# Kernel optimization log

Hardware: AMD Instinct MI355X
Metric: run time of the kernel (lower is better)

Reference implementation:

```python
import jax, jax.numpy as jnp
import numpy as np

L, D, H, T, B, V, R = 12, 1024, 16, 1024, 2, 50257, 32
HD = D // H
LORA_SCALE = 64.0 / 32.0  # alpha / rank
EPS = 1e-5


def setup_inputs() -> dict:
    key = jax.random.key(0)
    ks = iter(jax.random.split(key, 32))
    f = lambda shape, s=0.02: jax.random.normal(next(ks), shape, dtype=jnp.float32) * s
    inp = {
        'input_ids': jax.random.randint(next(ks), (B, T), 0, V, dtype=jnp.int64),
        'wte': f((V, D)), 'wpe': f((T, D)),
        'ln1_w': jnp.ones((L, D), jnp.float32), 'ln1_b': jnp.zeros((L, D), jnp.float32),
        'attn_w': f((L, 3 * D, D)), 'attn_b': jnp.zeros((L, 3 * D), jnp.float32),
        'attn_la': f((L, R, D), 0.01), 'attn_lb': f((L, 3 * D, R), 0.01),
        'proj_w': f((L, D, D)), 'proj_b': jnp.zeros((L, D), jnp.float32),
        'proj_la': f((L, R, D), 0.01), 'proj_lb': f((L, D, R), 0.01),
        'ln2_w': jnp.ones((L, D), jnp.float32), 'ln2_b': jnp.zeros((L, D), jnp.float32),
        'fc_w': f((L, 4 * D, D)), 'fc_b': jnp.zeros((L, 4 * D), jnp.float32),
        'fc_la': f((L, R, D), 0.01), 'fc_lb': f((L, 4 * D, R), 0.01),
        'mp_w': f((L, D, 4 * D)), 'mp_b': jnp.zeros((L, D), jnp.float32),
        'mp_la': f((L, R, 4 * D), 0.01), 'mp_lb': f((L, D, R), 0.01),
        'lnf_w': jnp.ones((D,), jnp.float32), 'lnf_b': jnp.zeros((D,), jnp.float32),
    }
    return inp


def _ln(x, w, b):
    m = jnp.mean(x, axis=-1, keepdims=True)
    v = jnp.mean(jnp.square(x - m), axis=-1, keepdims=True)
    return (x - m) * jax.lax.rsqrt(v + EPS) * w + b


def _lin(x, W, b, A, Bm):
    # quantized linear at 32-bit (pass-through) + LoRA: x W^T + b + scale * (x A^T) B^T
    return x @ W.T + b + ((x @ A.T) @ Bm.T) * LORA_SCALE


def _forward(input_ids, wte, wpe, ln1_w, ln1_b, attn_w, attn_b, attn_la, attn_lb,
             proj_w, proj_b, proj_la, proj_lb, ln2_w, ln2_b, fc_w, fc_b, fc_la, fc_lb,
             mp_w, mp_b, mp_la, mp_lb, lnf_w, lnf_b):
    Bq, Tq = input_ids.shape
    mask = jnp.tril(jnp.ones((Tq, Tq), dtype=bool))  # causal bias buffer
    h = wte[input_ids] + wpe[jnp.arange(Tq)]  # embed + (eval-mode) dropout

    def blk(h, p):
        l1w, l1b, aw, ab, ala, alb, pw, pb, pla, plb, l2w, l2b, fw, fb, fla, flb, mw, mb, mla, mlb = p
        x = _ln(h, l1w, l1b)
        qkv = _lin(x, aw, ab, ala, alb)  # [B,T,3D]
        q, k, v = jnp.split(qkv, 3, axis=-1)
        q = q.reshape(Bq, Tq, H, HD).transpose(0, 2, 1, 3)
        k = k.reshape(Bq, Tq, H, HD).transpose(0, 2, 1, 3)
        v = v.reshape(Bq, Tq, H, HD).transpose(0, 2, 1, 3)
        s = jnp.einsum('bhqd,bhkd->bhqk', q, k) / jnp.sqrt(jnp.float32(HD))
        s = jnp.where(mask, s, -jnp.inf)
        pa = jax.nn.softmax(s, axis=-1)
        o = jnp.einsum('bhqk,bhkd->bhqd', pa, v).transpose(0, 2, 1, 3).reshape(Bq, Tq, D)
        h = h + _lin(o, pw, pb, pla, plb)
        x = _ln(h, l2w, l2b)
        m = jax.nn.gelu(_lin(x, fw, fb, fla, flb), approximate=False)
        h = h + _lin(m, mw, mb, mla, mlb)
        return h, None

    h, _ = jax.lax.scan(blk, h, (ln1_w, ln1_b, attn_w, attn_b, attn_la, attn_lb,
                                 proj_w, proj_b, proj_la, proj_lb, ln2_w, ln2_b,
                                 fc_w, fc_b, fc_la, fc_lb, mp_w, mp_b, mp_la, mp_lb))
    return _ln(h, lnf_w, lnf_b)


def reference(input_ids, wte, wpe, ln1_w, ln1_b, attn_w, attn_b, attn_la, attn_lb,
              proj_w, proj_b, proj_la, proj_lb, ln2_w, ln2_b, fc_w, fc_b, fc_la, fc_lb,
              mp_w, mp_b, mp_la, mp_lb, lnf_w, lnf_b):
    return _forward(input_ids, wte, wpe, ln1_w, ln1_b, attn_w, attn_b, attn_la, attn_lb,
                    proj_w, proj_b, proj_la, proj_lb, ln2_w, ln2_b, fc_w, fc_b, fc_la, fc_lb,
                    mp_w, mp_b, mp_la, mp_lb, lnf_w, lnf_b)
```

## Files before the change

kernel.cpp:

```cpp
#include <hip/hip_runtime.h>
#include <math.h>

#define TT 1024
#define DD 1024
#define NH 16
#define NB 2
#define NL 12
#define RR 32
#define MM (NB * TT)

typedef __attribute__((ext_vector_type(8))) short bf16x8;
typedef __attribute__((ext_vector_type(4))) float f32x4;

__device__ __forceinline__ unsigned short f2bf(float f) {
  unsigned int u = __float_as_uint(f);
  u = (u + 0x7FFFu + ((u >> 16) & 1u)) >> 16;
  return (unsigned short)u;
}
__device__ __forceinline__ float bf2f(unsigned short u) {
  return __uint_as_float((unsigned int)u << 16);
}

typedef __attribute__((address_space(1))) void gvoid;
typedef __attribute__((address_space(3))) void lvoid;
__device__ __forceinline__ void gload_lds16(const void* g, void* l) {
  __builtin_amdgcn_global_load_lds((gvoid*)g, (lvoid*)l, 16, 0, 0);
}

__global__ __launch_bounds__(256) void embed_cvt_k(
    const int* __restrict__ ids, const float* __restrict__ wte,
    const float* __restrict__ wpe, float* __restrict__ h,
    const float* __restrict__ ala, const float* __restrict__ alb,
    const float* __restrict__ pla, const float* __restrict__ plb,
    const float* __restrict__ fla, const float* __restrict__ flb,
    const float* __restrict__ mla, const float* __restrict__ mlb,
    unsigned short* __restrict__ out) {
  if (blockIdx.x < MM * DD / 256) {
    const int i = blockIdx.x * 256 + threadIdx.x;
    const int row = i >> 10;
    const int d = i & 1023;
    const int t = row & (TT - 1);
    const int id = ids[row];
    h[i] = wte[(size_t)id * DD + d] + wpe[(size_t)t * DD + d];
    return;
  }
  const int g = (blockIdx.x - MM * DD / 256) * 256 + threadIdx.x;
  const int layer = g >> 19;
  const int rem = g & 524287;
  const int row = rem >> 5;
  const int r = rem & 31;
  float v;
  if (row < 1024)       v = ala[(size_t)layer * 32 * 1024 + r * 1024 + row];
  else if (row < 4096)  v = alb[(size_t)layer * 3072 * 32 + (row - 1024) * 32 + r];
  else if (row < 5120)  v = pla[(size_t)layer * 32 * 1024 + r * 1024 + (row - 4096)];
  else if (row < 6144)  v = plb[(size_t)layer * 1024 * 32 + (row - 5120) * 32 + r];
  else if (row < 7168)  v = fla[(size_t)layer * 32 * 1024 + r * 1024 + (row - 6144)];
  else if (row < 11264) v = flb[(size_t)layer * 4096 * 32 + (row - 7168) * 32 + r];
  else if (row < 15360) v = mla[(size_t)layer * 32 * 4096 + r * 4096 + (row - 11264)];
  else                  v = mlb[(size_t)layer * 1024 * 32 + (row - 15360) * 32 + r];
  out[g] = f2bf(v);
}

__global__ __launch_bounds__(256) void ln_bf_k(const float* __restrict__ x,
                                               const float* __restrict__ w,
                                               const float* __restrict__ b,
                                               unsigned short* __restrict__ out) {
  const int row = blockIdx.x;
  const float* xr = x + (size_t)row * DD;
  const float4 v = *(const float4*)(xr + threadIdx.x * 4);
  float s = v.x + v.y + v.z + v.w;
  float ss = v.x * v.x + v.y * v.y + v.z * v.z + v.w * v.w;
#pragma unroll
  for (int off = 32; off > 0; off >>= 1) {
    s += __shfl_down(s, off);
    ss += __shfl_down(ss, off);
  }
  __shared__ float rs[4], rss[4];
  const int wid = threadIdx.x >> 6;
  if ((threadIdx.x & 63) == 0) { rs[wid] = s; rss[wid] = ss; }
  __syncthreads();
  s = rs[0] + rs[1] + rs[2] + rs[3];
  ss = rss[0] + rss[1] + rss[2] + rss[3];
  const float mean = s * (1.f / DD);
  const float var = ss * (1.f / DD) - mean * mean;
  const float rstd = rsqrtf(var + 1e-5f);
  const float4 wv = *(const float4*)(w + threadIdx.x * 4);
  const float4 bv = *(const float4*)(b + threadIdx.x * 4);
  ushort4 o;
  o.x = f2bf((v.x - mean) * rstd * wv.x + bv.x);
  o.y = f2bf((v.y - mean) * rstd * wv.y + bv.y);
  o.z = f2bf((v.z - mean) * rstd * wv.z + bv.z);
  o.w = f2bf((v.w - mean) * rstd * wv.w + bv.w);
  *(ushort4*)(out + (size_t)row * DD + threadIdx.x * 4) = o;
}

__global__ __launch_bounds__(256) void ln_f_k(const float* __restrict__ x,
                                              const float* __restrict__ w,
                                              const float* __restrict__ b,
                                              float* __restrict__ out) {
  const int row = blockIdx.x;
  const float* xr = x + (size_t)row * DD;
  const float4 v = *(const float4*)(xr + threadIdx.x * 4);
  float s = v.x + v.y + v.z + v.w;
  float ss = v.x * v.x + v.y * v.y + v.z * v.z + v.w * v.w;
#pragma unroll
  for (int off = 32; off > 0; off >>= 1) {
    s += __shfl_down(s, off);
    ss += __shfl_down(ss, off);
  }
  __shared__ float rs[4], rss[4];
  const int wid = threadIdx.x >> 6;
  if ((threadIdx.x & 63) == 0) { rs[wid] = s; rss[wid] = ss; }
  __syncthreads();
  s = rs[0] + rs[1] + rs[2] + rs[3];
  ss = rss[0] + rss[1] + rss[2] + rss[3];
  const float mean = s * (1.f / DD);
  const float var = ss * (1.f / DD) - mean * mean;
  const float rstd = rsqrtf(var + 1e-5f);
  const float4 wv = *(const float4*)(w + threadIdx.x * 4);
  const float4 bv = *(const float4*)(b + threadIdx.x * 4);
  float4 o;
  o.x = (v.x - mean) * rstd * wv.x + bv.x;
  o.y = (v.y - mean) * rstd * wv.y + bv.y;
  o.z = (v.z - mean) * rstd * wv.z + bv.z;
  o.w = (v.w - mean) * rstd * wv.w + bv.w;
  *(float4*)(out + (size_t)row * DD + threadIdx.x * 4) = o;
}

__global__ __launch_bounds__(256) void fold_ln_k(
    const float* __restrict__ aw, const float* __restrict__ pw,
    const float* __restrict__ fw, const float* __restrict__ mw,
    const unsigned short* __restrict__ Lb,
    unsigned short* __restrict__ oq, unsigned short* __restrict__ op_,
    unsigned short* __restrict__ of, unsigned short* __restrict__ om,
    const float* __restrict__ hln, const float* __restrict__ lnw,
    const float* __restrict__ lnb, unsigned short* __restrict__ xout) {
  __shared__ unsigned short dl[64 * 128];
  const int tid = threadIdx.x;
  if (blockIdx.x >= 1536) {
    const int row = blockIdx.x - 1536;
    const float* xr = hln + (size_t)row * DD;
    const float4 v = *(const float4*)(xr + tid * 4);
    float s = v.x + v.y + v.z + v.w;
    float ss = v.x * v.x + v.y * v.y + v.z * v.z + v.w * v.w;
#pragma unroll
    for (int off = 32; off > 0; off >>= 1) {
      s += __shfl_down(s, off);
      ss += __shfl_down(ss, off);
    }
    float* red = (float*)dl;
    const int wid = tid >> 6;
    if ((tid & 63) == 0) { red[wid] = s; red[4 + wid] = ss; }
    __syncthreads();
    s = red[0] + red[1] + red[2] + red[3];
    ss = red[4] + red[5] + red[6] + red[7];
    const float mean = s * (1.f / DD);
    const float var = ss * (1.f / DD) - mean * mean;
    const float rstd = rsqrtf(var + 1e-5f);
    const float4 wv = *(const float4*)(lnw + tid * 4);
    const float4 bv = *(const float4*)(lnb + tid * 4);
    ushort4 o;
    o.x = f2bf((v.x - mean) * rstd * wv.x + bv.x);
    o.y = f2bf((v.y - mean) * rstd * wv.y + bv.y);
    o.z = f2bf((v.z - mean) * rstd * wv.z + bv.z);
    o.w = f2bf((v.w - mean) * rstd * wv.w + bv.w);
    *(ushort4*)(xout + (size_t)row * DD + tid * 4) = o;
    return;
  }
  const int lid = blockIdx.x;
  const float* W;
  unsigned short* out;
  const unsigned short *Bl, *Al;
  int K, n0, kblk;
  if (lid < 384) {
    W = aw; out = oq; Bl = Lb + 1024 * 32; Al = Lb;
    K = DD; n0 = (lid >> 3) * 64; kblk = (lid & 7) * 128;
  } else if (lid < 512) {
    const int t = lid - 384;
    W = pw; out = op_; Bl = Lb + 5120 * 32; Al = Lb + 4096 * 32;
    K = DD; n0 = (t >> 3) * 64; kblk = (t & 7) * 128;
  } else if (lid < 1024) {
    const int t = lid - 512;
    W = fw; out = of; Bl = Lb + 7168 * 32; Al = Lb + 6144 * 32;
    K = DD; n0 = (t >> 3) * 64; kblk = (t & 7) * 128;
  } else {
    const int t = lid - 1024;
    W = mw; out = om; Bl = Lb + 15360 * 32; Al = Lb + 11264 * 32;
    K = 4 * DD; n0 = (t >> 5) * 64; kblk = (t & 31) * 128;
  }
  const int w = tid >> 6, l = tid & 63;
  const int lr16 = l & 15, lg = l >> 4;
  const int nloc = w * 16 + lr16;
  const bf16x8 bfrag = *(const bf16x8*)(Bl + (size_t)(n0 + nloc) * 32 + lg * 8);
#pragma unroll
  for (int kc = 0; kc < 8; ++kc) {
    const bf16x8 afr = *(const bf16x8*)(Al + (size_t)(kblk + kc * 16 + lr16) * 32 + lg * 8);
    f32x4 acc = {};
    acc = __builtin_amdgcn_mfma_f32_16x16x32_bf16(afr, bfrag, acc, 0, 0, 0);
    ushort4 dv;
    dv.x = f2bf(2.f * acc[0]); dv.y = f2bf(2.f * acc[1]);
    dv.z = f2bf(2.f * acc[2]); dv.w = f2bf(2.f * acc[3]);
    const unsigned int byte = ((unsigned)(nloc * 256 + kc * 32 + lg * 8)) ^
                              (((unsigned)nloc & 3u) << 5);
    *(ushort4*)((char*)dl + byte) = dv;
  }
  __syncthreads();
  float4 wv[8];
#pragma unroll
  for (int it = 0; it < 8; ++it) {
    const int flat = it * 1024 + tid * 4;
    const int row = flat >> 7;
    const int k = flat & 127;
    wv[it] = *(const float4*)(W + (size_t)(n0 + row) * K + kblk + k);
  }
  asm volatile("s_waitcnt vmcnt(0)" ::: "memory");
#pragma unroll
  for (int it = 0; it < 8; ++it) {
    const int flat = it * 1024 + tid * 4;
    const int row = flat >> 7;
    const int k = flat & 127;
    const unsigned int byte = ((unsigned)(row * 256 + k * 2)) ^
                              (((unsigned)row & 3u) << 5);
    const ushort4 dv = *(const ushort4*)((const char*)dl + byte);
    ushort4 o;
    o.x = f2bf(wv[it].x + bf2f(dv.x));
    o.y = f2bf(wv[it].y + bf2f(dv.y));
    o.z = f2bf(wv[it].z + bf2f(dv.z));
    o.w = f2bf(wv[it].w + bf2f(dv.w));
    *(ushort4*)(out + (size_t)(n0 + row) * K + kblk + k) = o;
  }
}

template <int BMt, int BNt, int BKt, int MODE>
__global__ __launch_bounds__(256) void gemm_t(const unsigned short* __restrict__ A,
                                              const unsigned short* __restrict__ Wt,
                                              const float* __restrict__ bias,
                                              const float* __restrict__ res,
                                              float* __restrict__ Cf,
                                              unsigned short* __restrict__ Cb,
                                              unsigned short* __restrict__ vt,
                                              int M, int N, int K) {
  constexpr int MI2 = BMt / 32, NJ2 = BNt / 32;
  constexpr int SB = BKt * 2;
  constexpr int SL = BKt / 8;
  constexpr int RC = 1024 / SB;
  constexpr int CAw = BMt / RC / 4;
  constexpr int CBw = BNt / RC / 4;
  __shared__ unsigned short As[BMt * BKt];
  __shared__ unsigned short Bs[BNt * BKt];
  const int tid = threadIdx.x;
  const int w = tid >> 6, l = tid & 63;
  const int gx = gridDim.x;
  const int bid = blockIdx.y * gx + blockIdx.x;
  const int cpx = (gx * gridDim.y) >> 3;
  const int logical = (bid & 7) * cpx + (bid >> 3);
  const int bm = (logical / gx) * BMt, bn = (logical % gx) * BNt;
  const int wr = w >> 1, wc = w & 1;
  const int lr16 = l & 15, lg = l >> 4, l7 = l & 7;
  const int rin = l / SL;
  const int slot = l % SL;
  f32x4 acc[MI2][NJ2] = {};
  for (int k0 = 0; k0 < K; k0 += BKt) {
    __syncthreads();
#pragma unroll
    for (int i = 0; i < CAw; ++i) {
      const int ch = w * CAw + i;
      const int row = ch * RC + rin;
      gload_lds16(A + (size_t)(bm + row) * K + k0 + ((slot ^ (row & 7)) * 8),
                  (char*)As + ch * 1024);
    }
#pragma unroll
    for (int i = 0; i < CBw; ++i) {
      const int ch = w * CBw + i;
      const int row = ch * RC + rin;
      gload_lds16(Wt + (size_t)(bn + row) * K + k0 + ((slot ^ (row & 7)) * 8),
                  (char*)Bs + ch * 1024);
    }
    __syncthreads();
#pragma unroll
    for (int kk = 0; kk < BKt / 32; ++kk) {
      bf16x8 af[MI2], bfr[NJ2];
      const int q = (kk * 4 + lg) ^ l7;
#pragma unroll
      for (int mi = 0; mi < MI2; ++mi)
        af[mi] = *(const bf16x8*)((const char*)As +
            (wr * (BMt / 2) + mi * 16 + lr16) * SB + q * 16);
#pragma unroll
      for (int nj = 0; nj < NJ2; ++nj)
        bfr[nj] = *(const bf16x8*)((const char*)Bs +
            (wc * (BNt / 2) + nj * 16 + lr16) * SB + q * 16);
#pragma unroll
      for (int mi = 0; mi < MI2; ++mi)
#pragma unroll
        for (int nj = 0; nj < NJ2; ++nj)
          acc[mi][nj] = __builtin_amdgcn_mfma_f32_16x16x32_bf16(
              af[mi], bfr[nj], acc[mi][nj], 0, 0, 0);
    }
  }
  const int cr = lg * 4;
  const int cc = lr16;
#pragma unroll
  for (int mi = 0; mi < MI2; ++mi) {
    const int gr0 = bm + wr * (BMt / 2) + mi * 16 + cr;
#pragma unroll
    for (int nj = 0; nj < NJ2; ++nj) {
      const int gc = bn + wc * (BNt / 2) + nj * 16 + cc;
      const float bv = bias[gc];
      if (MODE == 3) {
        if (gc < 2048) {
#pragma unroll
          for (int r = 0; r < 4; ++r)
            Cb[(size_t)(gr0 + r) * 2048 + gc] = f2bf(acc[mi][nj][r] + bv);
        } else {
          const int hv = gc - 2048;
          const int b_ = gr0 >> 10, t0 = gr0 & 1023;
          ushort4 u;
          u.x = f2bf(acc[mi][nj][0] + bv); u.y = f2bf(acc[mi][nj][1] + bv);
          u.z = f2bf(acc[mi][nj][2] + bv); u.w = f2bf(acc[mi][nj][3] + bv);
          *(ushort4*)(vt + ((size_t)(b_ * 1024 + hv)) * 1024 + t0) = u;
        }
      } else if (MODE == 1) {
#pragma unroll
        for (int r = 0; r < 4; ++r) {
          const size_t idx = (size_t)(gr0 + r) * N + gc;
          Cf[idx] = acc[mi][nj][r] + bv + res[idx];
        }
      } else {
#pragma unroll
        for (int r = 0; r < 4; ++r) {
          float v = acc[mi][nj][r] + bv;
          v = 0.5f * v * (1.f + erff(v * 0.70710678118654752f));
          Cb[(size_t)(gr0 + r) * N + gc] = f2bf(v);
        }
      }
    }
  }
}

#define SM_SCALE_LOG2E 0.18033688011112042f
__global__ __launch_bounds__(256) void attn3_k(const unsigned short* __restrict__ qk,
                                               const unsigned short* __restrict__ vt,
                                               unsigned short* __restrict__ out) {
  const int qt = 15 - blockIdx.x;
  const int bh = blockIdx.y;
  const int b = bh >> 4, hh = bh & 15;
  const int tid = threadIdx.x;
  const int w = tid >> 6, l = tid & 63;
  const int lg = l >> 4;
  const int lr = l & 15;

  __shared__ unsigned short Kt[2][64 * 64];
  __shared__ unsigned short Vb[2][64 * 64];
  __shared__ unsigned short Pb[4][16 * 64];

  bf16x8 qf[2];
  {
    const unsigned short* qp =
        qk + ((size_t)(b * TT + qt * 64 + w * 16 + lr)) * 2048 + hh * 64 + lg * 8;
    qf[0] = *(const bf16x8*)(qp);
    qf[1] = *(const bf16x8*)(qp + 32);
  }
  f32x4 oacc[4] = {};
  float mrow[4] = {-1e30f, -1e30f, -1e30f, -1e30f};
  float lrow[4] = {0.f, 0.f, 0.f, 0.f};

  auto stage = [&](int buf, int kt) {
#pragma unroll
    for (int oo = 0; oo < 2; ++oo) {
      const int o = w + oo * 4;
      const int row = o * 8 + (l >> 3);
      const int sc = ((l & 7) ^ (l >> 3)) * 8;
      const unsigned short* ks =
          qk + ((size_t)(b * TT + kt * 64 + row)) * 2048 + 1024 + hh * 64 + sc;
      gload_lds16(ks, (char*)&Kt[buf][0] + o * 1024);
      const unsigned short* vs =
          vt + ((size_t)(bh * 64 + row)) * 1024 + kt * 64 + sc;
      gload_lds16(vs, (char*)&Vb[buf][0] + o * 1024);
    }
  };

  stage(0, 0);
  int cur = 0;
  unsigned short* Pw = &Pb[w][0];
  const int qlocal = w * 16 + lg * 4;

  for (int kt = 0; kt <= qt; ++kt) {
    __syncthreads();
    if (kt < qt) stage(cur ^ 1, kt + 1);
    const unsigned short* Kb_ = &Kt[cur][0];
    const unsigned short* Vb_ = &Vb[cur][0];
    const int effc = lr & 7;

    f32x4 s[4];
#pragma unroll
    for (int j = 0; j < 4; ++j) {
      f32x4 sj = {};
#pragma unroll
      for (int ks = 0; ks < 2; ++ks) {
        const bf16x8 kf = *(const bf16x8*)((const char*)Kb_ + (j * 16 + lr) * 128 +
                                           (((ks * 4 + lg) ^ effc) * 16));
        sj = __builtin_amdgcn_mfma_f32_16x16x32_bf16(qf[ks], kf, sj, 0, 0, 0);
      }
      s[j] = sj;
    }

    const bool last = (kt == qt);
    float tv[4][4];
#pragma unroll
    for (int j = 0; j < 4; ++j)
#pragma unroll
      for (int r = 0; r < 4; ++r) {
        float v = s[j][r] * SM_SCALE_LOG2E;
        if (last && (j * 16 + lr > qlocal + r)) v = -1e30f;
        tv[j][r] = v;
      }
    float corr[4];
#pragma unroll
    for (int r = 0; r < 4; ++r) {
      float mx = fmaxf(fmaxf(tv[0][r], tv[1][r]), fmaxf(tv[2][r], tv[3][r]));
      mx = fmaxf(mx, __shfl_xor(mx, 1));
      mx = fmaxf(mx, __shfl_xor(mx, 2));
      mx = fmaxf(mx, __shfl_xor(mx, 4));
      mx = fmaxf(mx, __shfl_xor(mx, 8));
      const float mn = fmaxf(mrow[r], mx);
      corr[r] = exp2f(mrow[r] - mn);
      mrow[r] = mn;
      lrow[r] *= corr[r];
    }
#pragma unroll
    for (int dt = 0; dt < 4; ++dt) {
      oacc[dt][0] *= corr[0]; oacc[dt][1] *= corr[1];
      oacc[dt][2] *= corr[2]; oacc[dt][3] *= corr[3];
    }
#pragma unroll
    for (int j = 0; j < 4; ++j)
#pragma unroll
      for (int r = 0; r < 4; ++r) {
        const float p = exp2f(tv[j][r] - mrow[r]);
        lrow[r] += p;
        const int q = lg * 4 + r;
        const int kv = j * 16 + lr;
        *(unsigned short*)((char*)Pw + q * 128 + ((kv * 2) ^ ((q & 7) << 4))) = f2bf(p);
      }
    asm volatile("s_waitcnt lgkmcnt(0)" ::: "memory");
    __builtin_amdgcn_sched_barrier(0);

#pragma unroll
    for (int ks = 0; ks < 2; ++ks) {
      const bf16x8 pf = *(const bf16x8*)((const char*)Pw + lr * 128 +
                                         (((ks * 4 + lg) ^ effc) * 16));
#pragma unroll
      for (int dt = 0; dt < 4; ++dt) {
        const bf16x8 vf = *(const bf16x8*)((const char*)Vb_ + (dt * 16 + lr) * 128 +
                                           (((ks * 4 + lg) ^ effc) * 16));
        oacc[dt] = __builtin_amdgcn_mfma_f32_16x16x32_bf16(pf, vf, oacc[dt], 0, 0, 0);
      }
    }
    cur ^= 1;
  }

#pragma unroll
  for (int r = 0; r < 4; ++r) {
    float lv = lrow[r];
    lv += __shfl_xor(lv, 1);
    lv += __shfl_xor(lv, 2);
    lv += __shfl_xor(lv, 4);
    lv += __shfl_xor(lv, 8);
    lrow[r] = 1.f / lv;
  }
  unsigned short* ob = out + ((size_t)(b * TT + qt * 64 + w * 16 + lg * 4)) * 1024 + hh * 64 + lr;
#pragma unroll
  for (int r = 0; r < 4; ++r)
#pragma unroll
    for (int dt = 0; dt < 4; ++dt)
      ob[(size_t)r * 1024 + dt * 16] = f2bf(oacc[dt][r] * lrow[r]);
}

extern "C" void kernel_launch(void* const* d_in, const int* in_sizes, int n_in,
                              void* d_out, int out_size, void* d_ws, size_t ws_size,
                              hipStream_t stream) {
  (void)in_sizes; (void)n_in; (void)out_size; (void)ws_size;
  const int* ids = (const int*)d_in[0];
  const float* wte = (const float*)d_in[1];
  const float* wpe = (const float*)d_in[2];
  const float* ln1w = (const float*)d_in[3];
  const float* ln1b = (const float*)d_in[4];
  const float* attnw = (const float*)d_in[5];
  const float* attnb = (const float*)d_in[6];
  const float* attnla = (const float*)d_in[7];
  const float* attnlb = (const float*)d_in[8];
  const float* projw = (const float*)d_in[9];
  const float* projb = (const float*)d_in[10];
  const float* projla = (const float*)d_in[11];
  const float* projlb = (const float*)d_in[12];
  const float* ln2w = (const float*)d_in[13];
  const float* ln2b = (const float*)d_in[14];
  const float* fcw = (const float*)d_in[15];
  const float* fcb = (const float*)d_in[16];
  const float* fcla = (const float*)d_in[17];
  const float* fclb = (const float*)d_in[18];
  const float* mpw = (const float*)d_in[19];
  const float* mpb = (const float*)d_in[20];
  const float* mpla = (const float*)d_in[21];
  const float* mplb = (const float*)d_in[22];
  const float* lnfw = (const float*)d_in[23];
  const float* lnfb = (const float*)d_in[24];

  char* ws = (char*)d_ws;
  float* h = (float*)ws;                        ws += (size_t)MM * DD * 4;
  unsigned short* x = (unsigned short*)ws;      ws += (size_t)MM * DD * 2;
  unsigned short* qkb = (unsigned short*)ws;    ws += (size_t)MM * 2 * DD * 2;
  unsigned short* vtb = (unsigned short*)ws;    ws += (size_t)MM * DD * 2;
  unsigned short* ho = (unsigned short*)ws;     ws += (size_t)MM * DD * 2;
  unsigned short* hm = (unsigned short*)ws;     ws += (size_t)MM * 4 * DD * 2;
  unsigned short* wqkv = (unsigned short*)ws;   ws += (size_t)3 * DD * DD * 2;
  unsigned short* wproj = (unsigned short*)ws;  ws += (size_t)DD * DD * 2;
  unsigned short* wfc = (unsigned short*)ws;    ws += (size_t)4 * DD * DD * 2;
  unsigned short* wmp = (unsigned short*)ws;    ws += (size_t)DD * 4 * DD * 2;
  unsigned short* loraP = (unsigned short*)ws;  ws += (size_t)NL * 16384 * 32 * 2;

  hipLaunchKernelGGL(embed_cvt_k, dim3(MM * DD / 256 + NL * 16384 * 32 / 256), dim3(256),
                     0, stream, ids, wte, wpe, h,
                     attnla, attnlb, projla, projlb, fcla, fclb, mpla, mplb, loraP);

  for (int l = 0; l < NL; ++l) {
    const float* ab = attnb + (size_t)l * 3 * DD;
    const float* pb = projb + (size_t)l * DD;
    const float* fb = fcb + (size_t)l * 4 * DD;
    const float* mb = mpb + (size_t)l * DD;

    hipLaunchKernelGGL(fold_ln_k, dim3(1536 + MM), dim3(256), 0, stream,
                       attnw + (size_t)l * 3 * DD * DD, projw + (size_t)l * DD * DD,
                       fcw + (size_t)l * 4 * DD * DD, mpw + (size_t)l * DD * 4 * DD,
                       loraP + (size_t)l * 16384 * 32, wqkv, wproj, wfc, wmp,
                       h, ln1w + (size_t)l * DD, ln1b + (size_t)l * DD, x);

    hipLaunchKernelGGL((gemm_t<128, 64, 128, 3>), dim3(3 * DD / 64, MM / 128), dim3(256), 0,
                       stream, x, wqkv, ab, (const float*)nullptr, (float*)nullptr,
                       qkb, vtb, MM, 3 * DD, DD);
    hipLaunchKernelGGL(attn3_k, dim3(TT / 64, NB * NH), dim3(256), 0, stream, qkb, vtb, ho);
    hipLaunchKernelGGL((gemm_t<64, 64, 256, 1>), dim3(DD / 64, MM / 64), dim3(256), 0,
                       stream, ho, wproj, pb, h, h, (unsigned short*)nullptr,
                       (unsigned short*)nullptr, MM, DD, DD);
    hipLaunchKernelGGL(ln_bf_k, dim3(MM), dim3(256), 0, stream, h,
                       ln2w + (size_t)l * DD, ln2b + (size_t)l * DD, x);
    hipLaunchKernelGGL((gemm_t<128, 128, 128, 2>), dim3(4 * DD / 128, MM / 128), dim3(256), 0,
                       stream, x, wfc, fb, (const float*)nullptr, (float*)nullptr, hm,
                       (unsigned short*)nullptr, MM, 4 * DD, DD);
    hipLaunchKernelGGL((gemm_t<64, 64, 256, 1>), dim3(DD / 64, MM / 64), dim3(256), 0,
                       stream, hm, wmp, mb, h, h, (unsigned short*)nullptr,
                       (unsigned short*)nullptr, MM, DD, 4 * DD);
  }

  hipLaunchKernelGGL(ln_f_k, dim3(MM), dim3(256), 0, stream, h, lnfw, lnfb, (float*)d_out);
}
```

Measured before the change: 1.785 ms.

## Widen attention key/value tiles to 128 and raise MFMA wave priority

The flash-attention kernel now processes 128 keys per iteration instead of 64. This halves the loop trip count and the number of barriers and softmax rescale steps, and the K, V and P shared-memory tiles grow to match with a 16-way XOR swizzle. MFMA sections are wrapped in s_setprio to favour matrix issue. In exchange, LDS use doubles, which may lower occupancy. The diagonal tile also now computes up to 64 fully masked keys for even query tiles.

```diff
diff --git a/kernel.cpp b/kernel.cpp
--- a/kernel.cpp
+++ b/kernel.cpp
@@ -113,7 +113,7 @@
   if ((threadIdx.x & 63) == 0) { rs[wid] = s; rss[wid] = ss; }
   __syncthreads();
   s = rs[0] + rs[1] + rs[2] + rs[3];
-  ss = rss[0] + rss[1] + rss[2] + rss[3];
+  ss = rss[4 - 4] + rss[1] + rss[2] + rss[3];
   const float mean = s * (1.f / DD);
   const float var = ss * (1.f / DD) - mean * mean;
   const float rstd = rsqrtf(var + 1e-5f);
@@ -338,7 +338,7 @@
 }
 
 #define SM_SCALE_LOG2E 0.18033688011112042f
-__global__ __launch_bounds__(256) void attn3_k(const unsigned short* __restrict__ qk,
+__global__ __launch_bounds__(256) void attn4_k(const unsigned short* __restrict__ qk,
                                                const unsigned short* __restrict__ vt,
                                                unsigned short* __restrict__ out) {
   const int qt = 15 - blockIdx.x;
@@ -349,9 +349,9 @@
   const int lg = l >> 4;
   const int lr = l & 15;
 
-  __shared__ unsigned short Kt[2][64 * 64];
-  __shared__ unsigned short Vb[2][64 * 64];
-  __shared__ unsigned short Pb[4][16 * 64];
+  __shared__ unsigned short Kt[2][128 * 64];
+  __shared__ unsigned short Vb[2][64 * 128];
+  __shared__ unsigned short Pb[4][16 * 128];
 
   bf16x8 qf[2];
   {
@@ -364,60 +364,69 @@
   float mrow[4] = {-1e30f, -1e30f, -1e30f, -1e30f};
   float lrow[4] = {0.f, 0.f, 0.f, 0.f};
 
-  auto stage = [&](int buf, int kt) {
-#pragma unroll
-    for (int oo = 0; oo < 2; ++oo) {
-      const int o = w + oo * 4;
-      const int row = o * 8 + (l >> 3);
+  auto stage = [&](int buf, int kt2) {
+#pragma unroll
+    for (int i = 0; i < 4; ++i) {
+      const int ch = w * 4 + i;
+      const int row = ch * 8 + (l >> 3);
       const int sc = ((l & 7) ^ (l >> 3)) * 8;
       const unsigned short* ks =
-          qk + ((size_t)(b * TT + kt * 64 + row)) * 2048 + 1024 + hh * 64 + sc;
-      gload_lds16(ks, (char*)&Kt[buf][0] + o * 1024);
+          qk + ((size_t)(b * TT + kt2 * 128 + row)) * 2048 + 1024 + hh * 64 + sc;
+      gload_lds16(ks, (char*)&Kt[buf][0] + ch * 1024);
+    }
+#pragma unroll
+    for (int i = 0; i < 4; ++i) {
+      const int ch = w * 4 + i;
+      const int row = ch * 4 + (l >> 4);
+      const int sc = ((l & 15) ^ (row & 15)) * 8;
       const unsigned short* vs =
-          vt + ((size_t)(bh * 64 + row)) * 1024 + kt * 64 + sc;
-      gload_lds16(vs, (char*)&Vb[buf][0] + o * 1024);
+          vt + ((size_t)(bh * 64 + row)) * 1024 + kt2 * 128 + sc;
+      gload_lds16(vs, (char*)&Vb[buf][0] + ch * 1024);
     }
   };
 
+  const int nkt = (qt >> 1) + 1;
   stage(0, 0);
   int cur = 0;
   unsigned short* Pw = &Pb[w][0];
   const int qlocal = w * 16 + lg * 4;
 
-  for (int kt = 0; kt <= qt; ++kt) {
+  for (int kt2 = 0; kt2 < nkt; ++kt2) {
     __syncthreads();
-    if (kt < qt) stage(cur ^ 1, kt + 1);
+    if (kt2 + 1 < nkt) stage(cur ^ 1, kt2 + 1);
     const unsigned short* Kb_ = &Kt[cur][0];
     const unsigned short* Vb_ = &Vb[cur][0];
-    const int effc = lr & 7;
-
-    f32x4 s[4];
-#pragma unroll
-    for (int j = 0; j < 4; ++j) {
+    const bool last = (kt2 == nkt - 1);
+
+    f32x4 s[8];
+    __builtin_amdgcn_s_setprio(1);
+#pragma unroll
+    for (int j = 0; j < 8; ++j) {
       f32x4 sj = {};
 #pragma unroll
       for (int ks = 0; ks < 2; ++ks) {
         const bf16x8 kf = *(const bf16x8*)((const char*)Kb_ + (j * 16 + lr) * 128 +
-                                           (((ks * 4 + lg) ^ effc) * 16));
+                                           (((ks * 4 + lg) ^ (lr & 7)) * 16));
         sj = __builtin_amdgcn_mfma_f32_16x16x32_bf16(qf[ks], kf, sj, 0, 0, 0);
       }
       s[j] = sj;
     }
-
-    const bool last = (kt == qt);
-    float tv[4][4];
-#pragma unroll
-    for (int j = 0; j < 4; ++j)
+    __builtin_amdgcn_s_setprio(0);
+
+#pragma unroll
+    for (int j = 0; j < 8; ++j)
 #pragma unroll
       for (int r = 0; r < 4; ++r) {
         float v = s[j][r] * SM_SCALE_LOG2E;
-        if (last && (j * 16 + lr > qlocal + r)) v = -1e30f;
-        tv[j][r] = v;
+        if (last && (kt2 * 128 + j * 16 + lr > qt * 64 + qlocal + r)) v = -1e30f;
+        s[j][r] = v;
       }
     float corr[4];
 #pragma unroll
     for (int r = 0; r < 4; ++r) {
-      float mx = fmaxf(fmaxf(tv[0][r], tv[1][r]), fmaxf(tv[2][r], tv[3][r]));
+      float mx = s[0][r];
+#pragma unroll
+      for (int j = 1; j < 8; ++j) mx = fmaxf(mx, s[j][r]);
       mx = fmaxf(mx, __shfl_xor(mx, 1));
       mx = fmaxf(mx, __shfl_xor(mx, 2));
       mx = fmaxf(mx, __shfl_xor(mx, 4));
@@ -433,29 +442,31 @@
       oacc[dt][2] *= corr[2]; oacc[dt][3] *= corr[3];
     }
 #pragma unroll
-    for (int j = 0; j < 4; ++j)
+    for (int j = 0; j < 8; ++j)
 #pragma unroll
       for (int r = 0; r < 4; ++r) {
-        const float p = exp2f(tv[j][r] - mrow[r]);
+        const float p = exp2f(s[j][r] - mrow[r]);
         lrow[r] += p;
         const int q = lg * 4 + r;
         const int kv = j * 16 + lr;
-        *(unsigned short*)((char*)Pw + q * 128 + ((kv * 2) ^ ((q & 7) << 4))) = f2bf(p);
+        *(unsigned short*)((char*)Pw + q * 256 + ((kv * 2) ^ ((q & 15) << 4))) = f2bf(p);
       }
     asm volatile("s_waitcnt lgkmcnt(0)" ::: "memory");
     __builtin_amdgcn_sched_barrier(0);
 
-#pragma unroll
-    for (int ks = 0; ks < 2; ++ks) {
-      const bf16x8 pf = *(const bf16x8*)((const char*)Pw + lr * 128 +
-                                         (((ks * 4 + lg) ^ effc) * 16));
+    __builtin_amdgcn_s_setprio(1);
+#pragma unroll
+    for (int ks = 0; ks < 4; ++ks) {
+      const bf16x8 pf = *(const bf16x8*)((const char*)Pw + lr * 256 +
+                                         (((ks * 4 + lg) ^ (lr & 15)) * 16));
 #pragma unroll
       for (int dt = 0; dt < 4; ++dt) {
-        const bf16x8 vf = *(const bf16x8*)((const char*)Vb_ + (dt * 16 + lr) * 128 +
-                                           (((ks * 4 + lg) ^ effc) * 16));
+        const bf16x8 vf = *(const bf16x8*)((const char*)Vb_ + (dt * 16 + lr) * 256 +
+                                           (((ks * 4 + lg) ^ (lr & 15)) * 16));
         oacc[dt] = __builtin_amdgcn_mfma_f32_16x16x32_bf16(pf, vf, oacc[dt], 0, 0, 0);
       }
     }
+    __builtin_amdgcn_s_setprio(0);
     cur ^= 1;
   }
 
@@ -538,7 +549,7 @@
     hipLaunchKernelGGL((gemm_t<128, 64, 128, 3>), dim3(3 * DD / 64, MM / 128), dim3(256), 0,
                        stream, x, wqkv, ab, (const float*)nullptr, (float*)nullptr,
                        qkb, vtb, MM, 3 * DD, DD);
-    hipLaunchKernelGGL(attn3_k, dim3(TT / 64, NB * NH), dim3(256), 0, stream, qkb, vtb, ho);
+    hipLaunchKernelGGL(attn4_k, dim3(TT / 64, NB * NH), dim3(256), 0, stream, qkb, vtb, ho);
     hipLaunchKernelGGL((gemm_t<64, 64, 256, 1>), dim3(DD / 64, MM / 64), dim3(256), 0,
                        stream, ho, wproj, pb, h, h, (unsigned short*)nullptr,
                        (unsigned short*)nullptr, MM, DD, DD);
```

New measurement: 1.742 ms. 2.4% less time.
